# Performance work log

Measured on AMD Instinct MI355X. Metric: run time of the kernel, lower is better.

Reference implementation:

```python
import jax, jax.numpy as jnp
import numpy as np

N = 50000   # nodes
E = 600000  # edges (before self loops)
D = 128     # in = hidden = out channels
EPS = 1e-5


def setup_inputs() -> dict:
    key = jax.random.key(0)
    ks = jax.random.split(key, 12)
    s = 1.0 / np.sqrt(D)
    inp = {
        "x": jax.random.normal(ks[0], (N, D), jnp.float32),
        "edge_index": jax.random.randint(ks[1], (2, E), 0, N, dtype=jnp.int64),
        "W1": jax.random.normal(ks[2], (D, D), jnp.float32) * s,
        "b1": jnp.zeros((D,), jnp.float32),
        "g1": jnp.ones((D,), jnp.float32),
        "be1": jnp.zeros((D,), jnp.float32),
        "W2": jax.random.normal(ks[3], (D, D), jnp.float32) * s,
        "b2": jnp.zeros((D,), jnp.float32),
        "g2": jnp.ones((D,), jnp.float32),
        "be2": jnp.zeros((D,), jnp.float32),
        "W3": jax.random.normal(ks[4], (D, D), jnp.float32) * s,
        "b3": jnp.zeros((D,), jnp.float32),
    }
    return inp


def _layer_norm(h, g, b):
    mu = jnp.mean(h, axis=-1, keepdims=True)
    var = jnp.mean(jnp.square(h - mu), axis=-1, keepdims=True)
    return (h - mu) * jax.lax.rsqrt(var + EPS) * g + b


def _gcn_layer(h, src, dst, ew, W, b, fill):
    # PyG gcn_norm: append internal self loops with weight `fill`
    loop = jnp.arange(N, dtype=src.dtype)
    s = jnp.concatenate([src, loop])
    d = jnp.concatenate([dst, loop])
    w = jnp.concatenate([ew, jnp.full((N,), fill, h.dtype)])
    deg = jax.ops.segment_sum(w, d, num_segments=N)
    dinv = jnp.where(deg > 0, jax.lax.rsqrt(deg), 0.0)
    norm = dinv[s] * w * dinv[d]  # [E_tot]
    hw = h @ W                    # [N, D]
    out = jax.ops.segment_sum(norm[:, None] * hw[s], d, num_segments=N)
    return out + b


def reference(x, edge_index, W1, b1, g1, be1, W2, b2, g2, be2, W3, b3):
    # outer add_self_loops with edge_weight = 1 (edge_attr is None path)
    loop = jnp.arange(N, dtype=edge_index.dtype)
    src = jnp.concatenate([edge_index[0], loop])
    dst = jnp.concatenate([edge_index[1], loop])
    ew = jnp.ones((E + N,), x.dtype)

    residual = x
    h = _gcn_layer(x, src, dst, ew, W1, b1, 2.0)   # improved=True
    h = jax.nn.relu(_layer_norm(h, g1, be1))
    h = _gcn_layer(h, src, dst, ew, W2, b2, 2.0)   # improved=True
    h = jax.nn.relu(_layer_norm(h, g2, be2))
    h = _gcn_layer(h, src, dst, ew, W3, b3, 1.0)   # improved=False
    return h + residual
```

## Files before the change

kernel.cpp:

```cpp
#include <hip/hip_runtime.h>
#include <hip/hip_bf16.h>
#include <cstdint>

#define N_NODES 50000
#define N_EDGES 600000
#define DCH     128
#define LN_EPS  1e-5f
#define SCAN_BLOCKS 196

typedef __attribute__((ext_vector_type(8))) __bf16 bf16x8;
typedef __attribute__((ext_vector_type(4))) float  f32x4;

__device__ inline unsigned short f2bf(float f) {
    unsigned int b; __builtin_memcpy(&b, &f, 4);
    b = b + 0x7fffu + ((b >> 16) & 1u);
    return (unsigned short)(b >> 16);
}
__device__ inline float bf_lo(unsigned int u) {
    unsigned int t = u << 16; float f; __builtin_memcpy(&f, &t, 4); return f;
}
__device__ inline float bf_hi(unsigned int u) {
    unsigned int t = u & 0xffff0000u; float f; __builtin_memcpy(&f, &t, 4); return f;
}

__global__ void detect_k(const int* __restrict__ ei, int* __restrict__ flag) {
    __shared__ int bad;
    if (threadIdx.x == 0) bad = 0;
    __syncthreads();
    const long long* e64 = (const long long*)ei;
    long long v = e64[threadIdx.x];
    long long w = e64[300000 + threadIdx.x];
    if (v < 0 || v >= N_NODES || w < 0 || w >= N_NODES) bad = 1;
    __syncthreads();
    if (threadIdx.x == 0) *flag = (bad == 0) ? 1 : 0;
}

__device__ inline int edge_at(const int* __restrict__ ei, int is64, long long idx) {
    long long v = is64 ? ((const long long*)ei)[idx] : (long long)ei[idx];
    if (v < 0) v = 0;
    if (v >= N_NODES) v = N_NODES - 1;
    return (int)v;
}


__global__ void count_k(const int* __restrict__ ei, const int* __restrict__ flag,
                        int* __restrict__ cnt) {
    int e = blockIdx.x * 256 + threadIdx.x;
    if (e < N_EDGES) {
        int d = edge_at(ei, *flag, (long long)N_EDGES + e);
        atomicAdd(&cnt[d], 1);
    }
}

__global__ void scan_block_k(const int* __restrict__ cnt, int* __restrict__ row_start,
                             int* __restrict__ bsums) {
    __shared__ int sm[256];
    int t = threadIdx.x;
    int i = blockIdx.x * 256 + t;
    int v = (i < N_NODES) ? cnt[i] : 0;
    sm[t] = v; __syncthreads();
    #pragma unroll
    for (int off = 1; off < 256; off <<= 1) {
        int x = (t >= off) ? sm[t - off] : 0;
        __syncthreads();
        sm[t] += x;
        __syncthreads();
    }
    if (i < N_NODES) row_start[i] = sm[t] - v;
    if (t == 255)    bsums[blockIdx.x] = sm[255];
}

__global__ void scan_top_k(int* __restrict__ bsums) {
    __shared__ int sm[256];
    int t = threadIdx.x;
    int v = (t < SCAN_BLOCKS) ? bsums[t] : 0;
    sm[t] = v; __syncthreads();
    #pragma unroll
    for (int off = 1; off < 256; off <<= 1) {
        int x = (t >= off) ? sm[t - off] : 0;
        __syncthreads();
        sm[t] += x;
        __syncthreads();
    }
    if (t < SCAN_BLOCKS) bsums[t] = sm[t] - v;
}

__global__ void finalize_k(const int* __restrict__ cnt, int* __restrict__ row_start,
                           int* __restrict__ cursor, const int* __restrict__ bsums,
                           float* __restrict__ dinv2, float* __restrict__ dinv1) {
    int i = blockIdx.x * 256 + threadIdx.x;
    if (i >= N_NODES) return;
    int rs = row_start[i] + bsums[blockIdx.x];
    row_start[i] = rs;
    cursor[i]    = rs;
    float c = (float)cnt[i];
    dinv2[i] = rsqrtf(c + 3.0f);
    dinv1[i] = rsqrtf(c + 2.0f);
}

__global__ void fill_k(const int* __restrict__ ei, const int* __restrict__ flag,
                       int* __restrict__ cursor, int* __restrict__ csr) {
    int e = blockIdx.x * 256 + threadIdx.x;
    if (e >= N_EDGES) return;
    int is64 = *flag;
    int s = edge_at(ei, is64, e);
    int d = edge_at(ei, is64, (long long)N_EDGES + e);
    int pos = atomicAdd(&cursor[d], 1);
    csr[pos] = s;
}

__global__ void cvt_x_k(const float* __restrict__ x, unsigned short* __restrict__ xbf) {
    int t = blockIdx.x * 256 + threadIdx.x;
    float4 v = *(const float4*)(x + (size_t)t * 4);
    unsigned int lo = ((unsigned int)f2bf(v.y) << 16) | (unsigned int)f2bf(v.x);
    unsigned int hi = ((unsigned int)f2bf(v.w) << 16) | (unsigned int)f2bf(v.z);
    uint2 r; r.x = lo; r.y = hi;
    *(uint2*)(xbf + (size_t)t * 4) = r;
}

__global__ void transpose_k(const float* __restrict__ W1,
                            const float* __restrict__ W2,
                            const float* __restrict__ W3,
                            unsigned short* __restrict__ Wt) {
    int t = blockIdx.x * 256 + threadIdx.x;
    int mat = t >> 14;
    int o = t & 16383;
    int n = o >> 7, k = o & 127;
    const float* W = (mat == 0) ? W1 : ((mat == 1) ? W2 : W3);
    Wt[t] = f2bf(W[k * 128 + n]);
}


__global__ __launch_bounds__(256) void agg_k(
        const unsigned short* __restrict__ h, unsigned short* __restrict__ out,
        const int* __restrict__ row_start, const int* __restrict__ cnt,
        const int* __restrict__ csr, const float* __restrict__ dinv, float fillp1) {
    int lane = threadIdx.x & 63;
    int node = blockIdx.x * 4 + (threadIdx.x >> 6);
    float di = dinv[node];
    int rs = row_start[node];
    int c  = cnt[node];
    const unsigned int* hp = (const unsigned int*)h + lane;
    float p0 = 0.f, p1 = 0.f, q0 = 0.f, q1 = 0.f;
    float r0 = 0.f, r1 = 0.f, s0 = 0.f, s1 = 0.f;
    int i = 0;
    for (; i + 4 <= c; i += 4) {
        int e0 = csr[rs + i], e1 = csr[rs + i + 1];
        int e2 = csr[rs + i + 2], e3 = csr[rs + i + 3];
        float w0 = dinv[e0], w1 = dinv[e1], w2 = dinv[e2], w3 = dinv[e3];
        unsigned int u0 = hp[(size_t)e0 * 64];
        unsigned int u1 = hp[(size_t)e1 * 64];
        unsigned int u2 = hp[(size_t)e2 * 64];
        unsigned int u3 = hp[(size_t)e3 * 64];
        p0 = fmaf(w0, bf_lo(u0), p0); p1 = fmaf(w0, bf_hi(u0), p1);
        q0 = fmaf(w1, bf_lo(u1), q0); q1 = fmaf(w1, bf_hi(u1), q1);
        r0 = fmaf(w2, bf_lo(u2), r0); r1 = fmaf(w2, bf_hi(u2), r1);
        s0 = fmaf(w3, bf_lo(u3), s0); s1 = fmaf(w3, bf_hi(u3), s1);
    }
    for (; i < c; i++) {
        int e = csr[rs + i];
        float w = dinv[e];
        unsigned int u = hp[(size_t)e * 64];
        p0 = fmaf(w, bf_lo(u), p0); p1 = fmaf(w, bf_hi(u), p1);
    }
    float a0 = (p0 + q0) + (r0 + s0);
    float a1 = (p1 + q1) + (r1 + s1);
    unsigned int us = hp[(size_t)node * 64];
    float dd = di * di * fillp1;
    a0 = di * a0 + dd * bf_lo(us);
    a1 = di * a1 + dd * bf_hi(us);
    unsigned int res = ((unsigned int)f2bf(a1) << 16) | (unsigned int)f2bf(a0);
    *((unsigned int*)out + (size_t)node * 64 + lane) = res;
}


template<int MODE>
__global__ __launch_bounds__(256) void gemm_k(
        const unsigned short* __restrict__ A,
        const unsigned short* __restrict__ Wt,
        const float* __restrict__ bias,
        const float* __restrict__ gamma,
        const float* __restrict__ beta,
        const float* __restrict__ resid,
        unsigned short* __restrict__ out_bf,
        float* __restrict__ out_f) {
    int lane = threadIdx.x & 63;
    int wv   = threadIdx.x >> 6;
    int r0   = (blockIdx.x * 4 + wv) * 16;
    int m = lane & 15, q = lane >> 4;

    int arow = r0 + m; if (arow >= N_NODES) arow = N_NODES - 1;
    const unsigned short* ap = A + (size_t)arow * DCH + q * 8;
    bf16x8 afr[4];
    #pragma unroll
    for (int kt = 0; kt < 4; kt++) afr[kt] = *(const bf16x8*)(ap + kt * 32);

    f32x4 acc[8];
    #pragma unroll
    for (int nt = 0; nt < 8; nt++) {
        f32x4 cacc = {0.f, 0.f, 0.f, 0.f};
        const unsigned short* bp = Wt + (size_t)(nt * 16 + m) * DCH + q * 8;
        #pragma unroll
        for (int kt = 0; kt < 4; kt++) {
            bf16x8 bfr = *(const bf16x8*)(bp + kt * 32);
            cacc = __builtin_amdgcn_mfma_f32_16x16x32_bf16(afr[kt], bfr, cacc, 0, 0, 0);
        }
        acc[nt] = cacc;
    }

    float bv[8];
    #pragma unroll
    for (int nt = 0; nt < 8; nt++) bv[nt] = bias[nt * 16 + m];

    if (MODE == 0) {
        float gv[8], bev[8];
        #pragma unroll
        for (int nt = 0; nt < 8; nt++) { gv[nt] = gamma[nt*16+m]; bev[nt] = beta[nt*16+m]; }
        #pragma unroll
        for (int nt = 0; nt < 8; nt++)
            #pragma unroll
            for (int r = 0; r < 4; r++) acc[nt][r] += bv[nt];
        #pragma unroll
        for (int r = 0; r < 4; r++) {
            float s = 0.f, qs = 0.f;
            #pragma unroll
            for (int nt = 0; nt < 8; nt++) { float v = acc[nt][r]; s += v; qs += v * v; }
            #pragma unroll
            for (int msk = 1; msk < 16; msk <<= 1) {
                s  += __shfl_xor(s,  msk, 16);
                qs += __shfl_xor(qs, msk, 16);
            }
            float mean = s * (1.f / 128.f);
            float var  = fmaxf(qs * (1.f / 128.f) - mean * mean, 0.f);
            float rstd = rsqrtf(var + LN_EPS);
            int row = r0 + q * 4 + r;
            if (row < N_NODES) {
                #pragma unroll
                for (int nt = 0; nt < 8; nt++) {
                    float v = (acc[nt][r] - mean) * rstd * gv[nt] + bev[nt];
                    out_bf[(size_t)row * DCH + nt * 16 + m] = f2bf(fmaxf(v, 0.f));
                }
            }
        }
    } else {
        #pragma unroll
        for (int r = 0; r < 4; r++) {
            int row = r0 + q * 4 + r;
            if (row < N_NODES) {
                #pragma unroll
                for (int nt = 0; nt < 8; nt++) {
                    float v = acc[nt][r] + bv[nt]
                            + resid[(size_t)row * DCH + nt * 16 + m];
                    out_f[(size_t)row * DCH + nt * 16 + m] = v;
                }
            }
        }
    }
}


extern "C" void kernel_launch(void* const* d_in, const int* in_sizes, int n_in,
                              void* d_out, int out_size, void* d_ws, size_t ws_size,
                              hipStream_t stream) {
    const float* x   = (const float*)d_in[0];
    const int*   ei  = (const int*)d_in[1];
    const float* W1  = (const float*)d_in[2];
    const float* b1  = (const float*)d_in[3];
    const float* g1  = (const float*)d_in[4];
    const float* be1 = (const float*)d_in[5];
    const float* W2  = (const float*)d_in[6];
    const float* b2  = (const float*)d_in[7];
    const float* g2  = (const float*)d_in[8];
    const float* be2 = (const float*)d_in[9];
    const float* W3  = (const float*)d_in[10];
    const float* b3  = (const float*)d_in[11];
    float* out = (float*)d_out;

    char* p = (char*)d_ws;
    auto alloc = [&](size_t bytes) -> void* {
        void* r = (void*)p; p += (bytes + 255) & ~(size_t)255; return r;
    };
    int*   eflag     = (int*)  alloc(256);
    int*   cnt       = (int*)  alloc((size_t)N_NODES * 4);
    int*   row_start = (int*)  alloc((size_t)N_NODES * 4);
    int*   cursor    = (int*)  alloc((size_t)N_NODES * 4);
    int*   bsums     = (int*)  alloc(256 * 4);
    float* dinv2     = (float*)alloc((size_t)N_NODES * 4);
    float* dinv1     = (float*)alloc((size_t)N_NODES * 4);
    int*   csr       = (int*)  alloc((size_t)N_EDGES * 4);
    unsigned short* Wt   = (unsigned short*)alloc((size_t)3 * 128 * 128 * 2);
    unsigned short* aggb = (unsigned short*)alloc((size_t)N_NODES * DCH * 2);
    unsigned short* hbuf = (unsigned short*)d_out;
    unsigned short* xbf  = hbuf + (size_t)N_NODES * DCH;

    hipMemsetAsync(cnt, 0, (size_t)N_NODES * 4, stream);
    detect_k<<<1, 256, 0, stream>>>(ei, eflag);
    count_k<<<(N_EDGES + 255) / 256, 256, 0, stream>>>(ei, eflag, cnt);
    scan_block_k<<<SCAN_BLOCKS, 256, 0, stream>>>(cnt, row_start, bsums);
    scan_top_k<<<1, 256, 0, stream>>>(bsums);
    finalize_k<<<SCAN_BLOCKS, 256, 0, stream>>>(cnt, row_start, cursor, bsums, dinv2, dinv1);
    fill_k<<<(N_EDGES + 255) / 256, 256, 0, stream>>>(ei, eflag, cursor, csr);
    cvt_x_k<<<(N_NODES * DCH / 4) / 256, 256, 0, stream>>>(x, xbf);
    transpose_k<<<192, 256, 0, stream>>>(W1, W2, W3, Wt);

    const int G_BLOCKS = (N_NODES + 63) / 64;

    agg_k<<<N_NODES / 4, 256, 0, stream>>>(xbf, aggb, row_start, cnt, csr, dinv2, 3.0f);
    gemm_k<0><<<G_BLOCKS, 256, 0, stream>>>(aggb, Wt, b1, g1, be1, nullptr, hbuf, nullptr);
    agg_k<<<N_NODES / 4, 256, 0, stream>>>(hbuf, aggb, row_start, cnt, csr, dinv2, 3.0f);
    gemm_k<0><<<G_BLOCKS, 256, 0, stream>>>(aggb, Wt + 16384, b2, g2, be2, nullptr, hbuf, nullptr);
    agg_k<<<N_NODES / 4, 256, 0, stream>>>(hbuf, aggb, row_start, cnt, csr, dinv1, 2.0f);
    gemm_k<1><<<G_BLOCKS, 256, 0, stream>>>(aggb, Wt + 32768, b3, nullptr, nullptr, x, nullptr, out);
}
```

Baseline: 340.3 us.

## Pre-scale features by dinv, pad CSR rows to eight, widen GEMM row tiles

Source-side normalisation (dinv[src]) is folded into the producer: x is pre-scaled in cvt_x_k, and the LayerNorm GEMM epilogue multiplies by the next layer's dinv. The aggregation therefore drops the per-edge dinv gather. CSR rows are padded to multiples of eight with a dummy zero node, which removes the tail loop and allows 8-way unrolled gathers, at the cost of extra padded loads and a larger CSR buffer with a fill kernel. The GEMM now processes 32 rows per wave so each B fragment is reused across two MFMAs.

Result: faster. 310.5 us (-8.8%).

```diff
diff --git a/kernel.cpp b/kernel.cpp
--- a/kernel.cpp
+++ b/kernel.cpp
@@ -7,6 +7,7 @@
 #define DCH     128
 #define LN_EPS  1e-5f
 #define SCAN_BLOCKS 196
+#define CSR_CAP 1000000
 
 typedef __attribute__((ext_vector_type(8))) __bf16 bf16x8;
 typedef __attribute__((ext_vector_type(4))) float  f32x4;
@@ -57,7 +58,7 @@
     __shared__ int sm[256];
     int t = threadIdx.x;
     int i = blockIdx.x * 256 + t;
-    int v = (i < N_NODES) ? cnt[i] : 0;
+    int v = (i < N_NODES) ? ((cnt[i] + 7) & ~7) : 0;
     sm[t] = v; __syncthreads();
     #pragma unroll
     for (int off = 1; off < 256; off <<= 1) {
@@ -98,6 +99,11 @@
     dinv1[i] = rsqrtf(c + 2.0f);
 }
 
+__global__ void pad_fill_k(int* __restrict__ csr) {
+    int i = blockIdx.x * 256 + threadIdx.x;
+    if (i < CSR_CAP) csr[i] = N_NODES;
+}
+
 __global__ void fill_k(const int* __restrict__ ei, const int* __restrict__ flag,
                        int* __restrict__ cursor, int* __restrict__ csr) {
     int e = blockIdx.x * 256 + threadIdx.x;
@@ -109,13 +115,22 @@
     csr[pos] = s;
 }
 
-__global__ void cvt_x_k(const float* __restrict__ x, unsigned short* __restrict__ xbf) {
-    int t = blockIdx.x * 256 + threadIdx.x;
-    float4 v = *(const float4*)(x + (size_t)t * 4);
-    unsigned int lo = ((unsigned int)f2bf(v.y) << 16) | (unsigned int)f2bf(v.x);
-    unsigned int hi = ((unsigned int)f2bf(v.w) << 16) | (unsigned int)f2bf(v.z);
-    uint2 r; r.x = lo; r.y = hi;
-    *(uint2*)(xbf + (size_t)t * 4) = r;
+__global__ void cvt_x_k(const float* __restrict__ x, const float* __restrict__ dinv2,
+                        unsigned short* __restrict__ xbf) {
+    int idx = blockIdx.x * 256 + threadIdx.x;
+    int node = idx >> 5;
+    if (node > N_NODES) return;
+    int co = (idx & 31) * 4;
+    uint2 r;
+    if (node == N_NODES) {
+        r.x = 0u; r.y = 0u;
+    } else {
+        float4 v = *(const float4*)(x + (size_t)node * DCH + co);
+        float d = dinv2[node];
+        r.x = ((unsigned int)f2bf(v.y * d) << 16) | (unsigned int)f2bf(v.x * d);
+        r.y = ((unsigned int)f2bf(v.w * d) << 16) | (unsigned int)f2bf(v.z * d);
+    }
+    *(uint2*)(xbf + (size_t)node * DCH + co) = r;
 }
 
 __global__ void transpose_k(const float* __restrict__ W1,
@@ -132,44 +147,45 @@
 
 
 __global__ __launch_bounds__(256) void agg_k(
-        const unsigned short* __restrict__ h, unsigned short* __restrict__ out,
+        const unsigned short* __restrict__ hs, unsigned short* __restrict__ out,
         const int* __restrict__ row_start, const int* __restrict__ cnt,
         const int* __restrict__ csr, const float* __restrict__ dinv, float fillp1) {
     int lane = threadIdx.x & 63;
     int node = blockIdx.x * 4 + (threadIdx.x >> 6);
     float di = dinv[node];
     int rs = row_start[node];
-    int c  = cnt[node];
-    const unsigned int* hp = (const unsigned int*)h + lane;
-    float p0 = 0.f, p1 = 0.f, q0 = 0.f, q1 = 0.f;
-    float r0 = 0.f, r1 = 0.f, s0 = 0.f, s1 = 0.f;
-    int i = 0;
-    for (; i + 4 <= c; i += 4) {
-        int e0 = csr[rs + i], e1 = csr[rs + i + 1];
-        int e2 = csr[rs + i + 2], e3 = csr[rs + i + 3];
-        float w0 = dinv[e0], w1 = dinv[e1], w2 = dinv[e2], w3 = dinv[e3];
+    int pc = (cnt[node] + 7) & ~7;
+    const unsigned int* hp = (const unsigned int*)hs + lane;
+    float a00 = 0.f, a01 = 0.f, a10 = 0.f, a11 = 0.f;
+    float a20 = 0.f, a21 = 0.f, a30 = 0.f, a31 = 0.f;
+    float a40 = 0.f, a41 = 0.f, a50 = 0.f, a51 = 0.f;
+    float a60 = 0.f, a61 = 0.f, a70 = 0.f, a71 = 0.f;
+    for (int i = 0; i < pc; i += 8) {
+        int e0 = csr[rs+i+0], e1 = csr[rs+i+1], e2 = csr[rs+i+2], e3 = csr[rs+i+3];
+        int e4 = csr[rs+i+4], e5 = csr[rs+i+5], e6 = csr[rs+i+6], e7 = csr[rs+i+7];
         unsigned int u0 = hp[(size_t)e0 * 64];
         unsigned int u1 = hp[(size_t)e1 * 64];
         unsigned int u2 = hp[(size_t)e2 * 64];
         unsigned int u3 = hp[(size_t)e3 * 64];
-        p0 = fmaf(w0, bf_lo(u0), p0); p1 = fmaf(w0, bf_hi(u0), p1);
-        q0 = fmaf(w1, bf_lo(u1), q0); q1 = fmaf(w1, bf_hi(u1), q1);
-        r0 = fmaf(w2, bf_lo(u2), r0); r1 = fmaf(w2, bf_hi(u2), r1);
-        s0 = fmaf(w3, bf_lo(u3), s0); s1 = fmaf(w3, bf_hi(u3), s1);
-    }
-    for (; i < c; i++) {
-        int e = csr[rs + i];
-        float w = dinv[e];
-        unsigned int u = hp[(size_t)e * 64];
-        p0 = fmaf(w, bf_lo(u), p0); p1 = fmaf(w, bf_hi(u), p1);
-    }
-    float a0 = (p0 + q0) + (r0 + s0);
-    float a1 = (p1 + q1) + (r1 + s1);
+        unsigned int u4 = hp[(size_t)e4 * 64];
+        unsigned int u5 = hp[(size_t)e5 * 64];
+        unsigned int u6 = hp[(size_t)e6 * 64];
+        unsigned int u7 = hp[(size_t)e7 * 64];
+        a00 += bf_lo(u0); a01 += bf_hi(u0);
+        a10 += bf_lo(u1); a11 += bf_hi(u1);
+        a20 += bf_lo(u2); a21 += bf_hi(u2);
+        a30 += bf_lo(u3); a31 += bf_hi(u3);
+        a40 += bf_lo(u4); a41 += bf_hi(u4);
+        a50 += bf_lo(u5); a51 += bf_hi(u5);
+        a60 += bf_lo(u6); a61 += bf_hi(u6);
+        a70 += bf_lo(u7); a71 += bf_hi(u7);
+    }
+    float s0 = ((a00 + a10) + (a20 + a30)) + ((a40 + a50) + (a60 + a70));
+    float s1 = ((a01 + a11) + (a21 + a31)) + ((a41 + a51) + (a61 + a71));
     unsigned int us = hp[(size_t)node * 64];
-    float dd = di * di * fillp1;
-    a0 = di * a0 + dd * bf_lo(us);
-    a1 = di * a1 + dd * bf_hi(us);
-    unsigned int res = ((unsigned int)f2bf(a1) << 16) | (unsigned int)f2bf(a0);
+    s0 = di * (s0 + fillp1 * bf_lo(us));
+    s1 = di * (s1 + fillp1 * bf_hi(us));
+    unsigned int res = ((unsigned int)f2bf(s1) << 16) | (unsigned int)f2bf(s0);
     *((unsigned int*)out + (size_t)node * 64 + lane) = res;
 }
 
@@ -181,31 +197,36 @@
         const float* __restrict__ bias,
         const float* __restrict__ gamma,
         const float* __restrict__ beta,
+        const float* __restrict__ dnext,
         const float* __restrict__ resid,
         unsigned short* __restrict__ out_bf,
         float* __restrict__ out_f) {
     int lane = threadIdx.x & 63;
     int wv   = threadIdx.x >> 6;
-    int r0   = (blockIdx.x * 4 + wv) * 16;
+    int r0   = (blockIdx.x * 4 + wv) * 32;
     int m = lane & 15, q = lane >> 4;
 
-    int arow = r0 + m; if (arow >= N_NODES) arow = N_NODES - 1;
-    const unsigned short* ap = A + (size_t)arow * DCH + q * 8;
-    bf16x8 afr[4];
-    #pragma unroll
-    for (int kt = 0; kt < 4; kt++) afr[kt] = *(const bf16x8*)(ap + kt * 32);
-
-    f32x4 acc[8];
+    bf16x8 afr[2][4];
+    #pragma unroll
+    for (int mt = 0; mt < 2; mt++) {
+        int arow = r0 + mt * 16 + m; if (arow >= N_NODES) arow = N_NODES - 1;
+        const unsigned short* ap = A + (size_t)arow * DCH + q * 8;
+        #pragma unroll
+        for (int kt = 0; kt < 4; kt++) afr[mt][kt] = *(const bf16x8*)(ap + kt * 32);
+    }
+
+    f32x4 acc[2][8];
     #pragma unroll
     for (int nt = 0; nt < 8; nt++) {
-        f32x4 cacc = {0.f, 0.f, 0.f, 0.f};
+        f32x4 c0 = {0.f,0.f,0.f,0.f}, c1 = {0.f,0.f,0.f,0.f};
         const unsigned short* bp = Wt + (size_t)(nt * 16 + m) * DCH + q * 8;
         #pragma unroll
         for (int kt = 0; kt < 4; kt++) {
             bf16x8 bfr = *(const bf16x8*)(bp + kt * 32);
-            cacc = __builtin_amdgcn_mfma_f32_16x16x32_bf16(afr[kt], bfr, cacc, 0, 0, 0);
+            c0 = __builtin_amdgcn_mfma_f32_16x16x32_bf16(afr[0][kt], bfr, c0, 0, 0, 0);
+            c1 = __builtin_amdgcn_mfma_f32_16x16x32_bf16(afr[1][kt], bfr, c1, 0, 0, 0);
         }
-        acc[nt] = cacc;
+        acc[0][nt] = c0; acc[1][nt] = c1;
     }
 
     float bv[8];
@@ -217,44 +238,51 @@
         #pragma unroll
         for (int nt = 0; nt < 8; nt++) { gv[nt] = gamma[nt*16+m]; bev[nt] = beta[nt*16+m]; }
         #pragma unroll
-        for (int nt = 0; nt < 8; nt++)
+        for (int mt = 0; mt < 2; mt++) {
             #pragma unroll
-            for (int r = 0; r < 4; r++) acc[nt][r] += bv[nt];
-        #pragma unroll
-        for (int r = 0; r < 4; r++) {
-            float s = 0.f, qs = 0.f;
+            for (int nt = 0; nt < 8; nt++)
+                #pragma unroll
+                for (int r = 0; r < 4; r++) acc[mt][nt][r] += bv[nt];
             #pragma unroll
-            for (int nt = 0; nt < 8; nt++) { float v = acc[nt][r]; s += v; qs += v * v; }
-            #pragma unroll
-            for (int msk = 1; msk < 16; msk <<= 1) {
-                s  += __shfl_xor(s,  msk, 16);
-                qs += __shfl_xor(qs, msk, 16);
-            }
-            float mean = s * (1.f / 128.f);
-            float var  = fmaxf(qs * (1.f / 128.f) - mean * mean, 0.f);
-            float rstd = rsqrtf(var + LN_EPS);
-            int row = r0 + q * 4 + r;
-            if (row < N_NODES) {
+            for (int r = 0; r < 4; r++) {
+                float s = 0.f, qs = 0.f;
                 #pragma unroll
-                for (int nt = 0; nt < 8; nt++) {
-                    float v = (acc[nt][r] - mean) * rstd * gv[nt] + bev[nt];
-                    out_bf[(size_t)row * DCH + nt * 16 + m] = f2bf(fmaxf(v, 0.f));
+                for (int nt = 0; nt < 8; nt++) { float v = acc[mt][nt][r]; s += v; qs += v*v; }
+                #pragma unroll
+                for (int msk = 1; msk < 16; msk <<= 1) {
+                    s  += __shfl_xor(s,  msk, 16);
+                    qs += __shfl_xor(qs, msk, 16);
+                }
+                float mean = s * (1.f / 128.f);
+                float var  = fmaxf(qs * (1.f / 128.f) - mean * mean, 0.f);
+                float rstd = rsqrtf(var + LN_EPS);
+                int row = r0 + mt * 16 + q * 4 + r;
+                if (row < N_NODES) {
+                    float dscale = dnext[row];
+                    #pragma unroll
+                    for (int nt = 0; nt < 8; nt++) {
+                        float v = (acc[mt][nt][r] - mean) * rstd * gv[nt] + bev[nt];
+                        v = fmaxf(v, 0.f) * dscale;
+                        out_bf[(size_t)row * DCH + nt * 16 + m] = f2bf(v);
+                    }
                 }
             }
         }
     } else {
         #pragma unroll
-        for (int r = 0; r < 4; r++) {
-            int row = r0 + q * 4 + r;
-            if (row < N_NODES) {
-                #pragma unroll
-                for (int nt = 0; nt < 8; nt++) {
-                    float v = acc[nt][r] + bv[nt]
-                            + resid[(size_t)row * DCH + nt * 16 + m];
-                    out_f[(size_t)row * DCH + nt * 16 + m] = v;
+        for (int mt = 0; mt < 2; mt++)
+            #pragma unroll
+            for (int r = 0; r < 4; r++) {
+                int row = r0 + mt * 16 + q * 4 + r;
+                if (row < N_NODES) {
+                    #pragma unroll
+                    for (int nt = 0; nt < 8; nt++) {
+                        float v = acc[mt][nt][r] + bv[nt]
+                                + resid[(size_t)row * DCH + nt * 16 + m];
+                        out_f[(size_t)row * DCH + nt * 16 + m] = v;
+                    }
                 }
             }
-        }
     }
 }
 
@@ -287,28 +315,30 @@
     int*   bsums     = (int*)  alloc(256 * 4);
     float* dinv2     = (float*)alloc((size_t)N_NODES * 4);
     float* dinv1     = (float*)alloc((size_t)N_NODES * 4);
-    int*   csr       = (int*)  alloc((size_t)N_EDGES * 4);
+    int*   csr       = (int*)  alloc((size_t)CSR_CAP * 4);
     unsigned short* Wt   = (unsigned short*)alloc((size_t)3 * 128 * 128 * 2);
     unsigned short* aggb = (unsigned short*)alloc((size_t)N_NODES * DCH * 2);
-    unsigned short* hbuf = (unsigned short*)d_out;
-    unsigned short* xbf  = hbuf + (size_t)N_NODES * DCH;
+    unsigned short* xbf  = (unsigned short*)alloc((size_t)(N_NODES + 1) * DCH * 2);
+    unsigned short* hbuf = (unsigned short*)alloc((size_t)(N_NODES + 1) * DCH * 2);
 
     hipMemsetAsync(cnt, 0, (size_t)N_NODES * 4, stream);
+    hipMemsetAsync(hbuf + (size_t)N_NODES * DCH, 0, DCH * 2, stream);
     detect_k<<<1, 256, 0, stream>>>(ei, eflag);
     count_k<<<(N_EDGES + 255) / 256, 256, 0, stream>>>(ei, eflag, cnt);
     scan_block_k<<<SCAN_BLOCKS, 256, 0, stream>>>(cnt, row_start, bsums);
     scan_top_k<<<1, 256, 0, stream>>>(bsums);
     finalize_k<<<SCAN_BLOCKS, 256, 0, stream>>>(cnt, row_start, cursor, bsums, dinv2, dinv1);
+    pad_fill_k<<<(CSR_CAP + 255) / 256, 256, 0, stream>>>(csr);
     fill_k<<<(N_EDGES + 255) / 256, 256, 0, stream>>>(ei, eflag, cursor, csr);
-    cvt_x_k<<<(N_NODES * DCH / 4) / 256, 256, 0, stream>>>(x, xbf);
+    cvt_x_k<<<((N_NODES + 1) * 32 + 255) / 256, 256, 0, stream>>>(x, dinv2, xbf);
     transpose_k<<<192, 256, 0, stream>>>(W1, W2, W3, Wt);
 
-    const int G_BLOCKS = (N_NODES + 63) / 64;
+    const int G_BLOCKS = (N_NODES + 127) / 128;
 
     agg_k<<<N_NODES / 4, 256, 0, stream>>>(xbf, aggb, row_start, cnt, csr, dinv2, 3.0f);
-    gemm_k<0><<<G_BLOCKS, 256, 0, stream>>>(aggb, Wt, b1, g1, be1, nullptr, hbuf, nullptr);
+    gemm_k<0><<<G_BLOCKS, 256, 0, stream>>>(aggb, Wt, b1, g1, be1, dinv2, nullptr, hbuf, nullptr);
     agg_k<<<N_NODES / 4, 256, 0, stream>>>(hbuf, aggb, row_start, cnt, csr, dinv2, 3.0f);
-    gemm_k<0><<<G_BLOCKS, 256, 0, stream>>>(aggb, Wt + 16384, b2, g2, be2, nullptr, hbuf, nullptr);
+    gemm_k<0><<<G_BLOCKS, 256, 0, stream>>>(aggb, Wt + 16384, b2, g2, be2, dinv1, nullptr, hbuf, nullptr);
     agg_k<<<N_NODES / 4, 256, 0, stream>>>(hbuf, aggb, row_start, cnt, csr, dinv1, 2.0f);
-    gemm_k<1><<<G_BLOCKS, 256, 0, stream>>>(aggb, Wt + 32768, b3, nullptr, nullptr, x, nullptr, out);
-}
+    gemm_k<1><<<G_BLOCKS, 256, 0, stream>>>(aggb, Wt + 32768, b3, nullptr, nullptr, nullptr, x, nullptr, out);
+}
```
